# Optimization experiments

Measured on AMD Instinct MI355X. Metric: run time of the kernel, lower is better.

Reference implementation:

```python
import jax, jax.numpy as jnp
import numpy as np
import math

B, S, D, H, L, FF = 16, 512, 1024, 16, 4, 4096
DK = D // H
EPS = 1e-5
NEG = -1e32


def make_pe(max_len, d_model):
    pos = np.arange(max_len, dtype=np.float32)[:, None]
    div = np.exp(np.arange(0, d_model, 2, dtype=np.float32) * (-math.log(10000.0) / d_model))
    pe = np.zeros((max_len, d_model), dtype=np.float32)
    pe[:, 0::2] = np.sin(pos * div)
    pe[:, 1::2] = np.cos(pos * div)
    return jnp.asarray(pe[None])  # [1, max_len, d_model]


def setup_inputs() -> dict:
    key = jax.random.key(0)
    ks = jax.random.split(key, 32)
    sd = 0.02
    inp = {
        'q_embed_data': jax.random.normal(ks[0], (B, S, D), jnp.float32),
        'qa_embed_data': jax.random.normal(ks[1], (B, S, D), jnp.float32),
        'forget_rate': jax.random.uniform(ks[2], (B, 1, S, 1), jnp.float32),
        'pe': make_pe(S, D),
        'Wk': jax.random.normal(ks[3], (L, D, D), jnp.float32) * sd,
        'bk': jnp.zeros((L, D), jnp.float32),
        'Wv': jax.random.normal(ks[4], (L, D, D), jnp.float32) * sd,
        'bv': jnp.zeros((L, D), jnp.float32),
        'Wo': jax.random.normal(ks[5], (L, D, D), jnp.float32) * sd,
        'bo': jnp.zeros((L, D), jnp.float32),
        'W1': jax.random.normal(ks[6], (L, D, FF), jnp.float32) * sd,
        'b1': jnp.zeros((L, FF), jnp.float32),
        'W2': jax.random.normal(ks[7], (L, FF, D), jnp.float32) * sd,
        'b2': jnp.zeros((L, D), jnp.float32),
        'ln1_g': jnp.ones((L, D), jnp.float32),
        'ln1_b': jnp.zeros((L, D), jnp.float32),
        'ln2_g': jnp.ones((L, D), jnp.float32),
        'ln2_b': jnp.zeros((L, D), jnp.float32),
    }
    return inp


def layernorm(x, g, b):
    m = jnp.mean(x, -1, keepdims=True)
    v = jnp.mean((x - m) ** 2, -1, keepdims=True)
    return (x - m) * jax.lax.rsqrt(v + EPS) * g + b


def forward(q_embed_data, qa_embed_data, forget_rate, pe,
            Wk, bk, Wv, bv, Wo, bo, W1, b1, W2, b2,
            ln1_g, ln1_b, ln2_g, ln2_b):
    x = q_embed_data + pe[:, :S]
    y = qa_embed_data + pe[:, :S]
    # mask==0 path: allowed positions are strictly below diagonal (j < i)
    allowed = jnp.tril(jnp.ones((S, S), bool), k=-1)
    scale = 1.0 / math.sqrt(DK)
    for l in range(L):
        # kq_same: q also uses k_linear
        k = (x @ Wk[l] + bk[l]).reshape(B, S, H, DK).transpose(0, 2, 1, 3)
        q = k
        v = (y @ Wv[l] + bv[l]).reshape(B, S, H, DK).transpose(0, 2, 1, 3)
        scores = jnp.einsum('bhid,bhjd->bhij', q, k) * scale
        scores = scores * forget_rate  # [B,1,S,1] broadcasts over heads/cols
        scores = jnp.where(allowed, scores, NEG)
        attn = jax.nn.softmax(scores, axis=-1)
        attn = attn.at[:, :, 0, :].set(0.0)  # zero_pad of first query row
        out = jnp.einsum('bhij,bhjd->bhid', attn, v)
        out = out.transpose(0, 2, 1, 3).reshape(B, S, D) @ Wo[l] + bo[l]
        x = layernorm(x + out, ln1_g[l], ln1_b[l])
        ff = jax.nn.relu(x @ W1[l] + b1[l]) @ W2[l] + b2[l]
        x = layernorm(x + ff, ln2_g[l], ln2_b[l])
    return x


def reference(q_embed_data, qa_embed_data, forget_rate, pe,
              Wk, bk, Wv, bv, Wo, bo, W1, b1, W2, b2,
              ln1_g, ln1_b, ln2_g, ln2_b):
    return forward(q_embed_data, qa_embed_data, forget_rate, pe,
                   Wk, bk, Wv, bv, Wo, bo, W1, b1, W2, b2,
                   ln1_g, ln1_b, ln2_g, ln2_b)
```

## Files before the change

### kernel.cpp

```cpp
#include <hip/hip_runtime.h>
#include <hip/hip_bf16.h>
#include <cstdint>
#include <cstddef>

#define Bq 16
#define Sq 512
#define Dq 1024
#define Hq 16
#define Lq 4
#define FFq 4096
#define Mq (Bq * Sq)

typedef unsigned short ushort_t;
typedef __attribute__((ext_vector_type(8))) short short8;
typedef __attribute__((ext_vector_type(8))) unsigned short ushortx8;
typedef __attribute__((ext_vector_type(4))) unsigned short ushortx4;
typedef __attribute__((ext_vector_type(4))) float floatx4;

__device__ __forceinline__ float bf2f(ushort_t u) {
  union { unsigned int i; float f; } x;
  x.i = ((unsigned int)u) << 16;
  return x.f;
}
__device__ __forceinline__ ushort_t f2bf(float f) {
  unsigned int u = __float_as_uint(f);
  u += 0x7fffu + ((u >> 16) & 1u);
  return (ushort_t)(u >> 16);
}

#define GLL16(gp, lp) __builtin_amdgcn_global_load_lds( \
    (__attribute__((address_space(1))) void*)(gp),      \
    (__attribute__((address_space(3))) void*)(lp), 16, 0, 0)

__global__ void probe_kernel(const ushort_t* __restrict__ pe,
                             const ushort_t* __restrict__ g1,
                             int* __restrict__ flags)
{
  if (threadIdx.x == 0 && blockIdx.x == 0) {
    flags[0] = (pe[1] == (ushort_t)0x3F80u) ? 1 : 0;
    flags[1] = (g1[0] == (ushort_t)0x3F80u) ? 1 : 0;
  }
}

struct CvtArgs {
  const void* src[10];
  ushort_t*   dst[10];
  int         n[10];
  int         fi[10];
  int         cum[11];
};
__global__ __launch_bounds__(256) void convert_all_kernel(
    CvtArgs a, const int* __restrict__ flags)
{
  const int bidx = blockIdx.x;
  int s = 0;
  while (s < 9 && bidx >= a.cum[s + 1]) ++s;
  const int i = (bidx - a.cum[s]) * 256 + threadIdx.x;
  if (i >= a.n[s]) return;
  if (flags[a.fi[s]]) a.dst[s][i] = ((const ushort_t*)a.src[s])[i];
  else                a.dst[s][i] = f2bf(((const float*)a.src[s])[i]);
}

__global__ __launch_bounds__(256) void gemm_bt_kernel(
    const ushort_t* __restrict__ A0, const ushort_t* __restrict__ BT0,
    const ushort_t* __restrict__ bias0, ushort_t* __restrict__ C0,
    const ushort_t* __restrict__ A1, const ushort_t* __restrict__ BT1,
    const ushort_t* __restrict__ bias1, ushort_t* __restrict__ C1,
    int N, int K, int relu)
{
  __shared__ __align__(16) ushort_t As[2][128 * 32];
  __shared__ __align__(16) ushort_t Bs[2][64 * 32];

  const ushort_t* A    = blockIdx.z ? A1 : A0;
  const ushort_t* BT   = blockIdx.z ? BT1 : BT0;
  const ushort_t* bias = blockIdx.z ? bias1 : bias0;
  ushort_t*       C    = blockIdx.z ? C1 : C0;

  const int t = threadIdx.x;
  const int lane = t & 63;
  const int w = t >> 6;
  const int la = lane & 15;
  const int lb = lane >> 4;

  int bx = blockIdx.x, by = blockIdx.y;
  {
    const int gx = gridDim.x, gy = gridDim.y;
    if ((gy & 7) == 0) {
      const int orig = by * gx + bx;
      const int xcd = orig & 7;
      const int local = orig >> 3;
      const int rows = gy >> 3;
      by = xcd * rows + local % rows;
      bx = local / rows;
    }
  }
  const long m0 = (long)by * 128;
  const long n0 = (long)bx * 64;
  const int nk = K >> 5;

  const int rA0 = t >> 2;
  const int rA1 = 64 + (t >> 2);
  const int cg  = t & 3;
  const int cA0 = (cg ^ ((rA0 >> 1) & 3)) << 3;
  const int cA1 = (cg ^ ((rA1 >> 1) & 3)) << 3;
  const ushort_t* gA0 = A + (m0 + rA0) * K + cA0;
  const ushort_t* gA1 = A + (m0 + rA1) * K + cA1;
  const ushort_t* gB0 = BT + (n0 + rA0) * K + cA0;
  const int loA0 = (w * 64) * 8;
  const int loA1 = (256 + w * 64) * 8;
  const int loB0 = (w * 64) * 8;

#define STAGE(buf, kt) do {                      \
    const long ko_ = (long)(kt) << 5;            \
    GLL16(gA0 + ko_, &As[(buf)][loA0]);          \
    GLL16(gA1 + ko_, &As[(buf)][loA1]);          \
    GLL16(gB0 + ko_, &Bs[(buf)][loB0]);          \
  } while (0)

  const floatx4 z4 = {0.f, 0.f, 0.f, 0.f};
  floatx4 acc[4][2];
#pragma unroll
  for (int i = 0; i < 4; ++i)
#pragma unroll
    for (int j = 0; j < 2; ++j) acc[i][j] = z4;

  STAGE(0, 0);
  __syncthreads();

  const int wm = (w >> 1) * 64;
  const int wn = (w & 1) * 32;
  int cur = 0;

  for (int kt = 0; kt < nk; ++kt) {
    if (kt + 1 < nk) STAGE(cur ^ 1, kt + 1);

    short8 af[4], bfr[2];
#pragma unroll
    for (int mf = 0; mf < 4; ++mf) {
      const int r = wm + mf * 16 + la;
      af[mf] = *(const short8*)&As[cur][r * 32 + ((lb ^ ((r >> 1) & 3)) << 3)];
    }
#pragma unroll
    for (int nf = 0; nf < 2; ++nf) {
      const int r = wn + nf * 16 + la;
      bfr[nf] = *(const short8*)&Bs[cur][r * 32 + ((lb ^ ((r >> 1) & 3)) << 3)];
    }
#pragma unroll
    for (int mf = 0; mf < 4; ++mf)
#pragma unroll
      for (int nf = 0; nf < 2; ++nf)
        acc[mf][nf] = __builtin_amdgcn_mfma_f32_16x16x32_bf16(af[mf], bfr[nf], acc[mf][nf], 0, 0, 0);

    __syncthreads();
    cur ^= 1;
  }
#undef STAGE

#pragma unroll
  for (int nf = 0; nf < 2; ++nf) {
    const long col = n0 + wn + nf * 16 + la;
    const float bsv = bf2f(bias[col]);
#pragma unroll
    for (int mf = 0; mf < 4; ++mf) {
      const long row = m0 + wm + mf * 16 + lb * 4;
      ushort_t* cp = C + row * N + col;
      const floatx4 v = acc[mf][nf];
#pragma unroll
      for (int r = 0; r < 4; ++r) {
        float x = v[r] + bsv;
        if (relu) x = fmaxf(x, 0.0f);
        cp[(long)r * N] = f2bf(x);
      }
    }
  }
}

__global__ __launch_bounds__(256) void attn_kernel(
    const ushort_t* __restrict__ kq, const ushort_t* __restrict__ vt,
    const ushort_t* __restrict__ fr, ushort_t* __restrict__ ao)
{
  __shared__ __align__(16) ushort_t P[4][64 * 72];
  const int t = threadIdx.x;
  const int lane = t & 63;
  const int w4 = t >> 6;
  const int wq = blockIdx.y * 4 + w4;
  const int b = blockIdx.x >> 4;
  const int h = blockIdx.x & 15;
  const int la = lane & 15;
  const int lb = lane >> 4;
  const int i0 = wq * 64;
  const long kbase = ((long)b * Sq) * Dq + h * 64;
  const long vbase = ((long)(b * Hq + h)) * (64L * Sq);

  short8 qf[4][2];
#pragma unroll
  for (int mf = 0; mf < 4; ++mf)
#pragma unroll
    for (int tt = 0; tt < 2; ++tt)
      qf[mf][tt] = *(const short8*)&kq[kbase + (long)(i0 + mf * 16 + la) * Dq + tt * 32 + lb * 8];

  float frs[4][4];
#pragma unroll
  for (int mf = 0; mf < 4; ++mf)
#pragma unroll
    for (int r = 0; r < 4; ++r)
      frs[mf][r] = 0.125f * bf2f(fr[b * Sq + i0 + mf * 16 + lb * 4 + r]);

  const floatx4 z4 = {0.f, 0.f, 0.f, 0.f};
  floatx4 o[4][4];
  float mrun[4][4], lrun[4][4];
#pragma unroll
  for (int mf = 0; mf < 4; ++mf)
#pragma unroll
    for (int x = 0; x < 4; ++x) {
      o[mf][x] = z4;
      mrun[mf][x] = -1e30f;
      lrun[mf][x] = 0.0f;
    }

  for (int jt = 0; jt <= wq; ++jt) {
    const int j0 = jt * 64;
    floatx4 s[4][4];
#pragma unroll
    for (int mf = 0; mf < 4; ++mf)
#pragma unroll
      for (int jf = 0; jf < 4; ++jf) s[mf][jf] = z4;

#pragma unroll
    for (int tt = 0; tt < 2; ++tt) {
      short8 kf[4];
#pragma unroll
      for (int jf = 0; jf < 4; ++jf)
        kf[jf] = *(const short8*)&kq[kbase + (long)(j0 + jf * 16 + la) * Dq + tt * 32 + lb * 8];
#pragma unroll
      for (int mf = 0; mf < 4; ++mf)
#pragma unroll
        for (int jf = 0; jf < 4; ++jf)
          s[mf][jf] = __builtin_amdgcn_mfma_f32_16x16x32_bf16(qf[mf][tt], kf[jf], s[mf][jf], 0, 0, 0);
    }

    const bool diag = (jt == wq);
#pragma unroll
    for (int mf = 0; mf < 4; ++mf)
#pragma unroll
      for (int jf = 0; jf < 4; ++jf)
#pragma unroll
        for (int r = 0; r < 4; ++r) {
          float x = s[mf][jf][r] * frs[mf][r];
          if (diag && (j0 + jf * 16 + la) >= (i0 + mf * 16 + lb * 4 + r)) x = -1e30f;
          s[mf][jf][r] = x;
        }

#pragma unroll
    for (int mf = 0; mf < 4; ++mf)
#pragma unroll
      for (int r = 0; r < 4; ++r) {
        float pm = fmaxf(fmaxf(s[mf][0][r], s[mf][1][r]), fmaxf(s[mf][2][r], s[mf][3][r]));
        pm = fmaxf(pm, __shfl_xor(pm, 1));
        pm = fmaxf(pm, __shfl_xor(pm, 2));
        pm = fmaxf(pm, __shfl_xor(pm, 4));
        pm = fmaxf(pm, __shfl_xor(pm, 8));
        const float mo = mrun[mf][r];
        const float mn = fmaxf(mo, pm);
        const float sc = __expf(mo - mn);
        mrun[mf][r] = mn;
        float rs = 0.0f;
#pragma unroll
        for (int jf = 0; jf < 4; ++jf) {
          const float p = __expf(s[mf][jf][r] - mn);
          s[mf][jf][r] = p;
          rs += p;
        }
        rs += __shfl_xor(rs, 1);
        rs += __shfl_xor(rs, 2);
        rs += __shfl_xor(rs, 4);
        rs += __shfl_xor(rs, 8);
        lrun[mf][r] = lrun[mf][r] * sc + rs;
#pragma unroll
        for (int df = 0; df < 4; ++df) o[mf][df][r] *= sc;
      }

#pragma unroll
    for (int mf = 0; mf < 4; ++mf)
#pragma unroll
      for (int jf = 0; jf < 4; ++jf)
#pragma unroll
        for (int r = 0; r < 4; ++r)
          P[w4][(mf * 16 + lb * 4 + r) * 72 + jf * 16 + la] = f2bf(s[mf][jf][r]);

#pragma unroll
    for (int tt = 0; tt < 2; ++tt) {
      short8 pf[4], vf[4];
#pragma unroll
      for (int mf = 0; mf < 4; ++mf)
        pf[mf] = *(const short8*)&P[w4][(mf * 16 + la) * 72 + tt * 32 + lb * 8];
#pragma unroll
      for (int df = 0; df < 4; ++df)
        vf[df] = *(const short8*)&vt[vbase + (long)(df * 16 + la) * Sq + j0 + tt * 32 + lb * 8];
#pragma unroll
      for (int mf = 0; mf < 4; ++mf)
#pragma unroll
        for (int df = 0; df < 4; ++df)
          o[mf][df] = __builtin_amdgcn_mfma_f32_16x16x32_bf16(pf[mf], vf[df], o[mf][df], 0, 0, 0);
    }
  }

#pragma unroll
  for (int mf = 0; mf < 4; ++mf)
#pragma unroll
    for (int df = 0; df < 4; ++df)
#pragma unroll
      for (int r = 0; r < 4; ++r) {
        const int ii = i0 + mf * 16 + lb * 4 + r;
        const float vv = (ii == 0) ? 0.0f : o[mf][df][r] / lrun[mf][r];
        ao[((long)b * Sq + ii) * Dq + h * 64 + df * 16 + la] = f2bf(vv);
      }
}

__global__ __launch_bounds__(256) void ln_kernel(
    float* __restrict__ xf, const ushort_t* __restrict__ add,
    const ushort_t* __restrict__ g, const ushort_t* __restrict__ bb,
    ushort_t* __restrict__ outb, float* __restrict__ outf,
    const int* __restrict__ flags, int final_)
{
  __shared__ float red[2][4];
  const long row = blockIdx.x;
  const int t = threadIdx.x;
  const int c = t * 4;
  float* xr = xf + row * Dq;
  const ushort_t* ar = add + row * Dq;

  floatx4 xv = *(floatx4*)&xr[c];
  ushortx4 av = *(const ushortx4*)&ar[c];
  float v[4];
  float s1 = 0.f, s2 = 0.f;
#pragma unroll
  for (int e = 0; e < 4; ++e) {
    v[e] = xv[e] + bf2f(av[e]);
    s1 += v[e];
    s2 += v[e] * v[e];
  }
#pragma unroll
  for (int m = 1; m < 64; m <<= 1) {
    s1 += __shfl_xor(s1, m);
    s2 += __shfl_xor(s2, m);
  }
  const int lane = t & 63, w = t >> 6;
  if (lane == 0) { red[0][w] = s1; red[1][w] = s2; }
  __syncthreads();
  s1 = red[0][0] + red[0][1] + red[0][2] + red[0][3];
  s2 = red[1][0] + red[1][1] + red[1][2] + red[1][3];
  const float mean = s1 * (1.0f / Dq);
  const float var = fmaxf(s2 * (1.0f / Dq) - mean * mean, 0.0f);
  const float rstd = rsqrtf(var + 1e-5f);
  ushortx4 gv = *(const ushortx4*)&g[c];
  ushortx4 bv = *(const ushortx4*)&bb[c];
  ushortx4 ob;
  floatx4 xo;
#pragma unroll
  for (int e = 0; e < 4; ++e) {
    const float y = (v[e] - mean) * rstd * bf2f(gv[e]) + bf2f(bv[e]);
    xo[e] = y;
    ob[e] = f2bf(y);
  }
  *(floatx4*)&xr[c] = xo;
  if (final_ && !flags[0]) {
    *(floatx4*)&outf[row * Dq + c] = xo;
  } else {
    *(ushortx4*)&outb[row * Dq + c] = ob;
  }
}

__global__ __launch_bounds__(256) void addpe_kernel(
    const void* __restrict__ qe, const void* __restrict__ qa,
    const void* __restrict__ pe, float* __restrict__ xf,
    ushort_t* __restrict__ xb, ushort_t* __restrict__ yb,
    const int* __restrict__ flags)
{
  const long i = ((long)blockIdx.x * 256 + threadIdx.x) * 8;
  const long sd = i & ((long)Sq * Dq - 1);
  const bool isb = flags[0] != 0;
  float q[8], a[8], p[8];
  if (isb) {
    ushortx8 q8 = *(const ushortx8*)((const ushort_t*)qe + i);
    ushortx8 a8 = *(const ushortx8*)((const ushort_t*)qa + i);
    ushortx8 p8 = *(const ushortx8*)((const ushort_t*)pe + sd);
#pragma unroll
    for (int e = 0; e < 8; ++e) { q[e] = bf2f(q8[e]); a[e] = bf2f(a8[e]); p[e] = bf2f(p8[e]); }
  } else {
    const float* qp = (const float*)qe + i;
    const float* ap = (const float*)qa + i;
    const float* pp = (const float*)pe + sd;
    floatx4 q0 = *(const floatx4*)qp, q1 = *(const floatx4*)(qp + 4);
    floatx4 a0 = *(const floatx4*)ap, a1 = *(const floatx4*)(ap + 4);
    floatx4 p0 = *(const floatx4*)pp, p1 = *(const floatx4*)(pp + 4);
#pragma unroll
    for (int e = 0; e < 4; ++e) {
      q[e] = q0[e]; q[e + 4] = q1[e];
      a[e] = a0[e]; a[e + 4] = a1[e];
      p[e] = p0[e]; p[e + 4] = p1[e];
    }
  }
  ushortx8 xo, yo;
  floatx4 f0, f1;
#pragma unroll
  for (int e = 0; e < 8; ++e) {
    const float xvv = (isb ? q[e] : bf2f(f2bf(q[e]))) + (isb ? p[e] : bf2f(f2bf(p[e])));
    const float yvv = (isb ? a[e] : bf2f(f2bf(a[e]))) + (isb ? p[e] : bf2f(f2bf(p[e])));
    if (e < 4) { f0[e] = xvv; } else { f1[e - 4] = xvv; }
    xo[e] = f2bf(xvv);
    yo[e] = f2bf(yvv);
  }
  *(floatx4*)&xf[i] = f0;
  *(floatx4*)&xf[i + 4] = f1;
  *(ushortx8*)&xb[i] = xo;
  *(ushortx8*)&yb[i] = yo;
}

__global__ __launch_bounds__(256) void transpose_kernel(
    const void* __restrict__ src, ushort_t* __restrict__ dst, int K, int N,
    const int* __restrict__ flags)
{
  __shared__ __align__(16) ushort_t tile[64][72];
  const bool isb = flags[1] != 0;
  const long base = (long)blockIdx.z * K * N;
  const int k0 = blockIdx.y * 64, n0 = blockIdx.x * 64;
  const int t = threadIdx.x;
  const int r = t >> 3;
  const int cc = (t & 7) << 3;
#pragma unroll
  for (int it = 0; it < 2; ++it) {
    const int rr = r + it * 32;
    const long gi = base + (long)(k0 + rr) * N + n0 + cc;
    if (isb) {
      *(short8*)&tile[rr][cc] = *(const short8*)((const ushort_t*)src + gi);
    } else {
      const float* sf = (const float*)src + gi;
      floatx4 v0 = *(const floatx4*)sf;
      floatx4 v1 = *(const floatx4*)(sf + 4);
#pragma unroll
      for (int e = 0; e < 4; ++e) {
        tile[rr][cc + e] = f2bf(v0[e]);
        tile[rr][cc + 4 + e] = f2bf(v1[e]);
      }
    }
  }
  __syncthreads();
#pragma unroll
  for (int it = 0; it < 2; ++it) {
    const int rr = r + it * 32;
    short8 v;
#pragma unroll
    for (int e = 0; e < 8; ++e) v[e] = (short)tile[cc + e][rr];
    *(short8*)&dst[base + (long)(n0 + rr) * K + k0 + cc] = v;
  }
}

__global__ __launch_bounds__(256) void vtrans_kernel(
    const ushort_t* __restrict__ vb, ushort_t* __restrict__ vt)
{
  __shared__ __align__(16) ushort_t tile[64][72];
  const int b = blockIdx.y >> 4, h = blockIdx.y & 15;
  const int j0 = blockIdx.x * 64;
  const int t = threadIdx.x;
  const int r = t >> 3;
  const int cc = (t & 7) << 3;
#pragma unroll
  for (int it = 0; it < 2; ++it) {
    const int rr = r + it * 32;
    *(short8*)&tile[rr][cc] = *(const short8*)&vb[((long)b * Sq + j0 + rr) * Dq + h * 64 + cc];
  }
  __syncthreads();
#pragma unroll
  for (int it = 0; it < 2; ++it) {
    const int rr = r + it * 32;
    short8 v;
#pragma unroll
    for (int e = 0; e < 8; ++e) v[e] = (short)tile[cc + e][rr];
    *(short8*)&vt[((long)(b * Hq + h) * 64 + rr) * Sq + j0 + cc] = v;
  }
}

extern "C" void kernel_launch(void* const* d_in, const int* in_sizes, int n_in,
                              void* d_out, int out_size, void* d_ws, size_t ws_size,
                              hipStream_t stream)
{
  if (n_in < 18) return;
  const void* qe  = d_in[0];
  const void* qa  = d_in[1];
  const void* fr  = d_in[2];
  const void* pe  = d_in[3];
  const void* Wk  = d_in[4];
  const void* bk  = d_in[5];
  const void* Wv  = d_in[6];
  const void* bv  = d_in[7];
  const void* Wo  = d_in[8];
  const void* bo  = d_in[9];
  const void* W1  = d_in[10];
  const void* b1  = d_in[11];
  const void* W2  = d_in[12];
  const void* b2  = d_in[13];
  const void* g1  = d_in[14];
  const void* be1 = d_in[15];
  const void* g2  = d_in[16];
  const void* be2 = d_in[17];

  char* ws = (char*)d_ws;
  const size_t SM = 243269632L;
  const size_t NEED = SM + 114752L;
  if (ws_size < NEED) return;

  float*    xf   = (float*)   (ws + 0L);
  ushort_t* xb   = (ushort_t*)(ws + 33554432L);
  ushort_t* yb   = (ushort_t*)(ws + 50331648L);
  ushort_t* tmpD = (ushort_t*)(ws + 67108864L);
  ushort_t* WkT  = (ushort_t*)(ws + 83886080L);
  ushort_t* WvT  = (ushort_t*)(ws + 92274688L);
  ushort_t* WoT  = (ushort_t*)(ws + 100663296L);
  ushort_t* W1T  = (ushort_t*)(ws + 109051904L);
  ushort_t* W2T  = (ushort_t*)(ws + 142606336L);
  ushort_t* kb   = (ushort_t*)(ws + 176160768L);
  ushort_t* vbf  = (ushort_t*)(ws + 192937984L);
  ushort_t* vtb  = (ushort_t*)(ws + 209715200L);
  ushort_t* ff1  = kb;

  int*      flags = (int*)(ws + SM);
  ushort_t* frc  = (ushort_t*)(ws + SM + 64);
  ushort_t* bkc  = (ushort_t*)(ws + SM + 16448);
  ushort_t* bvc  = (ushort_t*)(ws + SM + 24640);
  ushort_t* boc  = (ushort_t*)(ws + SM + 32832);
  ushort_t* b1c  = (ushort_t*)(ws + SM + 41024);
  ushort_t* b2c  = (ushort_t*)(ws + SM + 73792);
  ushort_t* g1c  = (ushort_t*)(ws + SM + 81984);
  ushort_t* be1c = (ushort_t*)(ws + SM + 90176);
  ushort_t* g2c  = (ushort_t*)(ws + SM + 98368);
  ushort_t* be2c = (ushort_t*)(ws + SM + 106560);

  probe_kernel<<<1, 64, 0, stream>>>((const ushort_t*)pe, (const ushort_t*)g1, flags);

  {
    CvtArgs a;
    const void* srcs[10] = {fr, bk, bv, bo, b1, b2, g1, be1, g2, be2};
    ushort_t*   dsts[10] = {frc, bkc, bvc, boc, b1c, b2c, g1c, be1c, g2c, be2c};
    const int   ns[10]   = {8192, 4096, 4096, 4096, 16384, 4096, 4096, 4096, 4096, 4096};
    int cum = 0;
    for (int s = 0; s < 10; ++s) {
      a.src[s] = srcs[s]; a.dst[s] = dsts[s]; a.n[s] = ns[s];
      a.fi[s] = (s == 0) ? 0 : 1;
      a.cum[s] = cum;
      cum += (ns[s] + 255) / 256;
    }
    a.cum[10] = cum;
    convert_all_kernel<<<cum, 256, 0, stream>>>(a, flags);
  }

  transpose_kernel<<<dim3(16, 16, 4), 256, 0, stream>>>(Wk, WkT, 1024, 1024, flags);
  transpose_kernel<<<dim3(16, 16, 4), 256, 0, stream>>>(Wv, WvT, 1024, 1024, flags);
  transpose_kernel<<<dim3(16, 16, 4), 256, 0, stream>>>(Wo, WoT, 1024, 1024, flags);
  transpose_kernel<<<dim3(64, 16, 4), 256, 0, stream>>>(W1, W1T, 1024, 4096, flags);
  transpose_kernel<<<dim3(16, 64, 4), 256, 0, stream>>>(W2, W2T, 4096, 1024, flags);

  addpe_kernel<<<4096, 256, 0, stream>>>(qe, qa, pe, xf, xb, yb, flags);

  for (int l = 0; l < 4; ++l) {
    gemm_bt_kernel<<<dim3(16, 64, 2), 256, 0, stream>>>(
        xb, WkT + (long)l * 1048576, bkc + l * 1024, kb,
        yb, WvT + (long)l * 1048576, bvc + l * 1024, vbf,
        1024, 1024, 0);
    vtrans_kernel<<<dim3(8, 256), 256, 0, stream>>>(vbf, vtb);
    attn_kernel<<<dim3(256, 2), 256, 0, stream>>>(kb, vtb, frc, vbf);
    gemm_bt_kernel<<<dim3(16, 64, 1), 256, 0, stream>>>(
        vbf, WoT + (long)l * 1048576, boc + l * 1024, tmpD,
        vbf, WoT + (long)l * 1048576, boc + l * 1024, tmpD,
        1024, 1024, 0);
    ln_kernel<<<8192, 256, 0, stream>>>(xf, tmpD, g1c + l * 1024, be1c + l * 1024, xb, nullptr, flags, 0);
    gemm_bt_kernel<<<dim3(64, 64, 1), 256, 0, stream>>>(
        xb, W1T + (long)l * 4194304, b1c + l * 4096, ff1,
        xb, W1T + (long)l * 4194304, b1c + l * 4096, ff1,
        4096, 1024, 1);
    gemm_bt_kernel<<<dim3(16, 64, 1), 256, 0, stream>>>(
        ff1, W2T + (long)l * 4194304, b2c + l * 1024, tmpD,
        ff1, W2T + (long)l * 4194304, b2c + l * 1024, tmpD,
        1024, 4096, 0);
    if (l == 3) {
      ln_kernel<<<8192, 256, 0, stream>>>(xf, tmpD, g2c + l * 1024, be2c + l * 1024,
                                          (ushort_t*)d_out, (float*)d_out, flags, 1);
    } else {
      ln_kernel<<<8192, 256, 0, stream>>>(xf, tmpD, g2c + l * 1024, be2c + l * 1024,
                                          xb, nullptr, flags, 0);
    }
  }
}
```

Measured before the change: 1.790 ms.

## Replace GEMM with 8-wave 256xBN tiled kernel using ping-pong MFMA scheduling

```diff
diff --git a/kernel.cpp b/kernel.cpp
--- a/kernel.cpp
+++ b/kernel.cpp
@@ -31,6 +31,12 @@
 #define GLL16(gp, lp) __builtin_amdgcn_global_load_lds( \
     (__attribute__((address_space(1))) void*)(gp),      \
     (__attribute__((address_space(3))) void*)(lp), 16, 0, 0)
+
+template<int N> __device__ __forceinline__ void waitvm() {
+  if constexpr (N == 0)      asm volatile("s_waitcnt vmcnt(0)" ::: "memory");
+  else if constexpr (N == 6) asm volatile("s_waitcnt vmcnt(6)" ::: "memory");
+  else                       asm volatile("s_waitcnt vmcnt(8)" ::: "memory");
+}
 
 __global__ void probe_kernel(const ushort_t* __restrict__ pe,
                              const ushort_t* __restrict__ g1,
@@ -61,15 +67,29 @@
   else                a.dst[s][i] = f2bf(((const float*)a.src[s])[i]);
 }
 
-__global__ __launch_bounds__(256) void gemm_bt_kernel(
+template<int BN>
+__global__ __launch_bounds__(512) void gemm8p_kernel(
     const ushort_t* __restrict__ A0, const ushort_t* __restrict__ BT0,
     const ushort_t* __restrict__ bias0, ushort_t* __restrict__ C0,
     const ushort_t* __restrict__ A1, const ushort_t* __restrict__ BT1,
     const ushort_t* __restrict__ bias1, ushort_t* __restrict__ C1,
     int N, int K, int relu)
 {
-  __shared__ __align__(16) ushort_t As[2][128 * 32];
-  __shared__ __align__(16) ushort_t Bs[2][64 * 32];
+  constexpr int BM  = 256;
+  constexpr int CHA = 4;
+  constexpr int CHB = BN / 64;
+  constexpr int NVM = CHA + CHB;
+  constexpr int WC  = (BN == 256) ? 4 : 2;
+  constexpr int WR  = 8 / WC;
+  constexpr int WM  = BM / WR;
+  constexpr int WN  = BN / WC;
+  constexpr int MF  = WM / 16;
+  constexpr int NF  = WN / 16;
+  constexpr int MH  = MF / 2;
+  constexpr int NH  = NF / 2;
+
+  __shared__ __align__(16) ushort_t As[2][BM * 64];
+  __shared__ __align__(16) ushort_t Bs[2][BN * 64];
 
   const ushort_t* A    = blockIdx.z ? A1 : A0;
   const ushort_t* BT   = blockIdx.z ? BT1 : BT0;
@@ -78,9 +98,12 @@
 
   const int t = threadIdx.x;
   const int lane = t & 63;
-  const int w = t >> 6;
+  const int wid = t >> 6;
   const int la = lane & 15;
   const int lb = lane >> 4;
+  const int l7 = la & 7;
+  const int wr = wid / WC;
+  const int wc = wid % WC;
 
   int bx = blockIdx.x, by = blockIdx.y;
   {
@@ -94,75 +117,114 @@
       bx = local / rows;
     }
   }
-  const long m0 = (long)by * 128;
-  const long n0 = (long)bx * 64;
-  const int nk = K >> 5;
-
-  const int rA0 = t >> 2;
-  const int rA1 = 64 + (t >> 2);
-  const int cg  = t & 3;
-  const int cA0 = (cg ^ ((rA0 >> 1) & 3)) << 3;
-  const int cA1 = (cg ^ ((rA1 >> 1) & 3)) << 3;
-  const ushort_t* gA0 = A + (m0 + rA0) * K + cA0;
-  const ushort_t* gA1 = A + (m0 + rA1) * K + cA1;
-  const ushort_t* gB0 = BT + (n0 + rA0) * K + cA0;
-  const int loA0 = (w * 64) * 8;
-  const int loA1 = (256 + w * 64) * 8;
-  const int loB0 = (w * 64) * 8;
-
-#define STAGE(buf, kt) do {                      \
-    const long ko_ = (long)(kt) << 5;            \
-    GLL16(gA0 + ko_, &As[(buf)][loA0]);          \
-    GLL16(gA1 + ko_, &As[(buf)][loA1]);          \
-    GLL16(gB0 + ko_, &Bs[(buf)][loB0]);          \
+  const long m0 = (long)by * BM;
+  const long n0 = (long)bx * BN;
+  const int nkt = K >> 6;
+
+  const int srow = t >> 3;
+  const int scol = ((t & 7) ^ ((t >> 3) & 7)) << 3;
+  const ushort_t* sA = A + (m0 + srow) * K + scol;
+  const ushort_t* sB = BT + (n0 + srow) * K + scol;
+  const long chs = 64L * K;
+  const int ldsb = wid * 512;
+
+  const int cofs0 = ((0 * 4 + lb) ^ l7) << 3;
+  const int cofs1 = ((1 * 4 + lb) ^ l7) << 3;
+  const int arow = wr * WM + la;
+  const int brow = wc * WN + la;
+
+  floatx4 acc[MF][NF];
+#pragma unroll
+  for (int i = 0; i < MF; ++i)
+#pragma unroll
+    for (int j = 0; j < NF; ++j) acc[i][j] = (floatx4){0.f, 0.f, 0.f, 0.f};
+
+  short8 a[MH][2], b[NH][2];
+
+#define STG(kt_) do {                                                        \
+    const long ko_ = (long)(kt_) << 6;                                       \
+    ushort_t* asb = &As[(kt_) & 1][0];                                       \
+    ushort_t* bsb = &Bs[(kt_) & 1][0];                                       \
+    _Pragma("unroll")                                                        \
+    for (int c = 0; c < CHA; ++c) GLL16(sA + c * chs + ko_, asb + c * 4096 + ldsb); \
+    _Pragma("unroll")                                                        \
+    for (int c = 0; c < CHB; ++c) GLL16(sB + c * chs + ko_, bsb + c * 4096 + ldsb); \
   } while (0)
 
-  const floatx4 z4 = {0.f, 0.f, 0.f, 0.f};
-  floatx4 acc[4][2];
-#pragma unroll
-  for (int i = 0; i < 4; ++i)
-#pragma unroll
-    for (int j = 0; j < 2; ++j) acc[i][j] = z4;
-
-  STAGE(0, 0);
-  __syncthreads();
-
-  const int wm = (w >> 1) * 64;
-  const int wn = (w & 1) * 32;
-  int cur = 0;
-
-  for (int kt = 0; kt < nk; ++kt) {
-    if (kt + 1 < nk) STAGE(cur ^ 1, kt + 1);
-
-    short8 af[4], bfr[2];
-#pragma unroll
-    for (int mf = 0; mf < 4; ++mf) {
-      const int r = wm + mf * 16 + la;
-      af[mf] = *(const short8*)&As[cur][r * 32 + ((lb ^ ((r >> 1) & 3)) << 3)];
-    }
-#pragma unroll
-    for (int nf = 0; nf < 2; ++nf) {
-      const int r = wn + nf * 16 + la;
-      bfr[nf] = *(const short8*)&Bs[cur][r * 32 + ((lb ^ ((r >> 1) & 3)) << 3)];
-    }
-#pragma unroll
-    for (int mf = 0; mf < 4; ++mf)
-#pragma unroll
-      for (int nf = 0; nf < 2; ++nf)
-        acc[mf][nf] = __builtin_amdgcn_mfma_f32_16x16x32_bf16(af[mf], bfr[nf], acc[mf][nf], 0, 0, 0);
-
-    __syncthreads();
-    cur ^= 1;
-  }
-#undef STAGE
-
-#pragma unroll
-  for (int nf = 0; nf < 2; ++nf) {
-    const long col = n0 + wn + nf * 16 + la;
+#define RDA(mh_, bb_) do {                                                   \
+    _Pragma("unroll")                                                        \
+    for (int m2 = 0; m2 < MH; ++m2) {                                        \
+      const int r_ = arow + ((mh_) * MH + m2) * 16;                          \
+      a[m2][0] = *(const short8*)&As[bb_][r_ * 64 + cofs0];                  \
+      a[m2][1] = *(const short8*)&As[bb_][r_ * 64 + cofs1];                  \
+    } } while (0)
+
+#define RDB(nh_, bb_) do {                                                   \
+    _Pragma("unroll")                                                        \
+    for (int n2 = 0; n2 < NH; ++n2) {                                        \
+      const int r_ = brow + ((nh_) * NH + n2) * 16;                          \
+      b[n2][0] = *(const short8*)&Bs[bb_][r_ * 64 + cofs0];                  \
+      b[n2][1] = *(const short8*)&Bs[bb_][r_ * 64 + cofs1];                  \
+    } } while (0)
+
+#define MM(mh_, nh_) do {                                                    \
+    __builtin_amdgcn_s_setprio(1);                                           \
+    _Pragma("unroll")                                                        \
+    for (int m2 = 0; m2 < MH; ++m2)                                          \
+    _Pragma("unroll")                                                        \
+    for (int n2 = 0; n2 < NH; ++n2)                                          \
+    _Pragma("unroll")                                                        \
+    for (int kk = 0; kk < 2; ++kk)                                           \
+      acc[(mh_) * MH + m2][(nh_) * NH + n2] =                                \
+        __builtin_amdgcn_mfma_f32_16x16x32_bf16(                             \
+          a[m2][kk], b[n2][kk], acc[(mh_) * MH + m2][(nh_) * NH + n2], 0, 0, 0); \
+    __builtin_amdgcn_s_setprio(0);                                           \
+  } while (0)
+
+#define LGKM() do { asm volatile("s_waitcnt lgkmcnt(0)" ::: "memory");       \
+    __builtin_amdgcn_sched_barrier(0); } while (0)
+#define BAR() __builtin_amdgcn_s_barrier()
+
+  STG(0);
+  for (int kt = 0; kt < nkt; ++kt) {
+    const int bb = kt & 1;
+    if (kt + 1 < nkt) { STG(kt + 1); waitvm<NVM>(); }
+    else              { waitvm<0>(); }
+    BAR();
+    RDA(0, bb); RDB(0, bb);
+    LGKM();
+    MM(0, 0);
+    BAR();
+    RDB(1, bb);
+    BAR();
+    LGKM();
+    MM(0, 1);
+    BAR();
+    RDA(1, bb);
+    BAR();
+    LGKM();
+    MM(1, 1);
+    BAR();
+    RDB(0, bb);
+    BAR();
+    LGKM();
+    MM(1, 0);
+    BAR();
+  }
+#undef STG
+#undef RDA
+#undef RDB
+#undef MM
+#undef LGKM
+#undef BAR
+
+#pragma unroll
+  for (int nf = 0; nf < NF; ++nf) {
+    const long col = n0 + wc * WN + nf * 16 + la;
     const float bsv = bf2f(bias[col]);
 #pragma unroll
-    for (int mf = 0; mf < 4; ++mf) {
-      const long row = m0 + wm + mf * 16 + lb * 4;
+    for (int mf = 0; mf < MF; ++mf) {
+      const long row = m0 + wr * WM + mf * 16 + lb * 4;
       ushort_t* cp = C + row * N + col;
       const floatx4 v = acc[mf][nf];
 #pragma unroll
@@ -563,22 +625,22 @@
   addpe_kernel<<<4096, 256, 0, stream>>>(qe, qa, pe, xf, xb, yb, flags);
 
   for (int l = 0; l < 4; ++l) {
-    gemm_bt_kernel<<<dim3(16, 64, 2), 256, 0, stream>>>(
+    gemm8p_kernel<128><<<dim3(8, 32, 2), 512, 0, stream>>>(
         xb, WkT + (long)l * 1048576, bkc + l * 1024, kb,
         yb, WvT + (long)l * 1048576, bvc + l * 1024, vbf,
         1024, 1024, 0);
     vtrans_kernel<<<dim3(8, 256), 256, 0, stream>>>(vbf, vtb);
     attn_kernel<<<dim3(256, 2), 256, 0, stream>>>(kb, vtb, frc, vbf);
-    gemm_bt_kernel<<<dim3(16, 64, 1), 256, 0, stream>>>(
+    gemm8p_kernel<128><<<dim3(8, 32, 1), 512, 0, stream>>>(
         vbf, WoT + (long)l * 1048576, boc + l * 1024, tmpD,
         vbf, WoT + (long)l * 1048576, boc + l * 1024, tmpD,
         1024, 1024, 0);
     ln_kernel<<<8192, 256, 0, stream>>>(xf, tmpD, g1c + l * 1024, be1c + l * 1024, xb, nullptr, flags, 0);
-    gemm_bt_kernel<<<dim3(64, 64, 1), 256, 0, stream>>>(
+    gemm8p_kernel<256><<<dim3(16, 32, 1), 512, 0, stream>>>(
         xb, W1T + (long)l * 4194304, b1c + l * 4096, ff1,
         xb, W1T + (long)l * 4194304, b1c + l * 4096, ff1,
         4096, 1024, 1);
-    gemm_bt_kernel<<<dim3(16, 64, 1), 256, 0, stream>>>(
+    gemm8p_kernel<128><<<dim3(8, 32, 1), 512, 0, stream>>>(
         ff1, W2T + (long)l * 4194304, b2c + l * 1024, tmpD,
         ff1, W2T + (long)l * 4194304, b2c + l * 1024, tmpD,
         1024, 4096, 0);
```

After: 1.920 ms. 1.07x slower.

## Enlarge GEMM tile to 256x128 with explicit vmcnt-pipelined double buffering

Applied to the files above, without the earlier changes.

```diff
diff --git a/kernel.cpp b/kernel.cpp
--- a/kernel.cpp
+++ b/kernel.cpp
@@ -61,15 +61,15 @@
   else                a.dst[s][i] = f2bf(((const float*)a.src[s])[i]);
 }
 
-__global__ __launch_bounds__(256) void gemm_bt_kernel(
+__global__ __launch_bounds__(256, 2) void gemmw_kernel(
     const ushort_t* __restrict__ A0, const ushort_t* __restrict__ BT0,
     const ushort_t* __restrict__ bias0, ushort_t* __restrict__ C0,
     const ushort_t* __restrict__ A1, const ushort_t* __restrict__ BT1,
     const ushort_t* __restrict__ bias1, ushort_t* __restrict__ C1,
     int N, int K, int relu)
 {
-  __shared__ __align__(16) ushort_t As[2][128 * 32];
-  __shared__ __align__(16) ushort_t Bs[2][64 * 32];
+  __shared__ __align__(16) ushort_t As[2][256 * 32];
+  __shared__ __align__(16) ushort_t Bs[2][128 * 32];
 
   const ushort_t* A    = blockIdx.z ? A1 : A0;
   const ushort_t* BT   = blockIdx.z ? BT1 : BT0;
@@ -78,9 +78,11 @@
 
   const int t = threadIdx.x;
   const int lane = t & 63;
-  const int w = t >> 6;
+  const int wid = t >> 6;
   const int la = lane & 15;
   const int lb = lane >> 4;
+  const int wr = wid >> 1;
+  const int wc = wid & 1;
 
   int bx = blockIdx.x, by = blockIdx.y;
   {
@@ -94,75 +96,75 @@
       bx = local / rows;
     }
   }
-  const long m0 = (long)by * 128;
-  const long n0 = (long)bx * 64;
+  const long m0 = (long)by * 256;
+  const long n0 = (long)bx * 128;
   const int nk = K >> 5;
 
-  const int rA0 = t >> 2;
-  const int rA1 = 64 + (t >> 2);
-  const int cg  = t & 3;
-  const int cA0 = (cg ^ ((rA0 >> 1) & 3)) << 3;
-  const int cA1 = (cg ^ ((rA1 >> 1) & 3)) << 3;
-  const ushort_t* gA0 = A + (m0 + rA0) * K + cA0;
-  const ushort_t* gA1 = A + (m0 + rA1) * K + cA1;
-  const ushort_t* gB0 = BT + (n0 + rA0) * K + cA0;
-  const int loA0 = (w * 64) * 8;
-  const int loA1 = (256 + w * 64) * 8;
-  const int loB0 = (w * 64) * 8;
-
-#define STAGE(buf, kt) do {                      \
-    const long ko_ = (long)(kt) << 5;            \
-    GLL16(gA0 + ko_, &As[(buf)][loA0]);          \
-    GLL16(gA1 + ko_, &As[(buf)][loA1]);          \
-    GLL16(gB0 + ko_, &Bs[(buf)][loB0]);          \
+  const int rA = t >> 2;
+  const int scol = (((t & 3) ^ ((rA >> 1) & 3)) << 3);
+  const ushort_t* sA = A + (m0 + rA) * (long)K + scol;
+  const ushort_t* sB = BT + (n0 + rA) * (long)K + scol;
+  const long rs64 = 64L * (long)K;
+  const int lws = wid * 512;
+
+#define STG(buf_, kt_) do {                                  \
+    const long ko_ = (long)(kt_) << 5;                       \
+    GLL16(sA + ko_,            &As[(buf_)][lws]);            \
+    GLL16(sA + rs64 + ko_,     &As[(buf_)][2048 + lws]);     \
+    GLL16(sA + 2 * rs64 + ko_, &As[(buf_)][4096 + lws]);     \
+    GLL16(sA + 3 * rs64 + ko_, &As[(buf_)][6144 + lws]);     \
+    GLL16(sB + ko_,            &Bs[(buf_)][lws]);            \
+    GLL16(sB + rs64 + ko_,     &Bs[(buf_)][2048 + lws]);     \
   } while (0)
 
-  const floatx4 z4 = {0.f, 0.f, 0.f, 0.f};
-  floatx4 acc[4][2];
-#pragma unroll
-  for (int i = 0; i < 4; ++i)
-#pragma unroll
-    for (int j = 0; j < 2; ++j) acc[i][j] = z4;
-
-  STAGE(0, 0);
-  __syncthreads();
-
-  const int wm = (w >> 1) * 64;
-  const int wn = (w & 1) * 32;
-  int cur = 0;
+  floatx4 acc[8][4];
+#pragma unroll
+  for (int i = 0; i < 8; ++i)
+#pragma unroll
+    for (int j = 0; j < 4; ++j) acc[i][j] = (floatx4){0.f, 0.f, 0.f, 0.f};
+
+  const int cofs = ((lb ^ ((la >> 1) & 3)) << 3);
+  const int ar0 = wr * 128 + la;
+  const int br0 = wc * 64 + la;
+
+  STG(0, 0);
 
   for (int kt = 0; kt < nk; ++kt) {
-    if (kt + 1 < nk) STAGE(cur ^ 1, kt + 1);
-
-    short8 af[4], bfr[2];
-#pragma unroll
-    for (int mf = 0; mf < 4; ++mf) {
-      const int r = wm + mf * 16 + la;
-      af[mf] = *(const short8*)&As[cur][r * 32 + ((lb ^ ((r >> 1) & 3)) << 3)];
-    }
-#pragma unroll
-    for (int nf = 0; nf < 2; ++nf) {
-      const int r = wn + nf * 16 + la;
-      bfr[nf] = *(const short8*)&Bs[cur][r * 32 + ((lb ^ ((r >> 1) & 3)) << 3)];
-    }
-#pragma unroll
-    for (int mf = 0; mf < 4; ++mf)
-#pragma unroll
-      for (int nf = 0; nf < 2; ++nf)
-        acc[mf][nf] = __builtin_amdgcn_mfma_f32_16x16x32_bf16(af[mf], bfr[nf], acc[mf][nf], 0, 0, 0);
-
-    __syncthreads();
-    cur ^= 1;
-  }
-#undef STAGE
-
-#pragma unroll
-  for (int nf = 0; nf < 2; ++nf) {
-    const long col = n0 + wn + nf * 16 + la;
+    const int buf = kt & 1;
+    if (kt + 1 < nk) {
+      STG(buf ^ 1, kt + 1);
+      asm volatile("s_waitcnt vmcnt(6)" ::: "memory");
+    } else {
+      asm volatile("s_waitcnt vmcnt(0)" ::: "memory");
+    }
+    __builtin_amdgcn_s_barrier();
+    __builtin_amdgcn_sched_barrier(0);
+
+    short8 af[8], bf[4];
+#pragma unroll
+    for (int mf = 0; mf < 8; ++mf)
+      af[mf] = *(const short8*)&As[buf][(ar0 + mf * 16) * 32 + cofs];
+#pragma unroll
+    for (int nf = 0; nf < 4; ++nf)
+      bf[nf] = *(const short8*)&Bs[buf][(br0 + nf * 16) * 32 + cofs];
+
+#pragma unroll
+    for (int nf = 0; nf < 4; ++nf)
+#pragma unroll
+      for (int mf = 0; mf < 8; ++mf)
+        acc[mf][nf] = __builtin_amdgcn_mfma_f32_16x16x32_bf16(af[mf], bf[nf], acc[mf][nf], 0, 0, 0);
+
+    __builtin_amdgcn_s_barrier();
+  }
+#undef STG
+
+#pragma unroll
+  for (int nf = 0; nf < 4; ++nf) {
+    const long col = n0 + wc * 64 + nf * 16 + la;
     const float bsv = bf2f(bias[col]);
 #pragma unroll
-    for (int mf = 0; mf < 4; ++mf) {
-      const long row = m0 + wm + mf * 16 + lb * 4;
+    for (int mf = 0; mf < 8; ++mf) {
+      const long row = m0 + wr * 128 + mf * 16 + lb * 4;
       ushort_t* cp = C + row * N + col;
       const floatx4 v = acc[mf][nf];
 #pragma unroll
@@ -563,22 +565,22 @@
   addpe_kernel<<<4096, 256, 0, stream>>>(qe, qa, pe, xf, xb, yb, flags);
 
   for (int l = 0; l < 4; ++l) {
-    gemm_bt_kernel<<<dim3(16, 64, 2), 256, 0, stream>>>(
+    gemmw_kernel<<<dim3(8, 32, 2), 256, 0, stream>>>(
         xb, WkT + (long)l * 1048576, bkc + l * 1024, kb,
         yb, WvT + (long)l * 1048576, bvc + l * 1024, vbf,
         1024, 1024, 0);
     vtrans_kernel<<<dim3(8, 256), 256, 0, stream>>>(vbf, vtb);
     attn_kernel<<<dim3(256, 2), 256, 0, stream>>>(kb, vtb, frc, vbf);
-    gemm_bt_kernel<<<dim3(16, 64, 1), 256, 0, stream>>>(
+    gemmw_kernel<<<dim3(8, 32, 1), 256, 0, stream>>>(
         vbf, WoT + (long)l * 1048576, boc + l * 1024, tmpD,
         vbf, WoT + (long)l * 1048576, boc + l * 1024, tmpD,
         1024, 1024, 0);
     ln_kernel<<<8192, 256, 0, stream>>>(xf, tmpD, g1c + l * 1024, be1c + l * 1024, xb, nullptr, flags, 0);
-    gemm_bt_kernel<<<dim3(64, 64, 1), 256, 0, stream>>>(
+    gemmw_kernel<<<dim3(32, 32, 1), 256, 0, stream>>>(
         xb, W1T + (long)l * 4194304, b1c + l * 4096, ff1,
         xb, W1T + (long)l * 4194304, b1c + l * 4096, ff1,
         4096, 1024, 1);
-    gemm_bt_kernel<<<dim3(16, 64, 1), 256, 0, stream>>>(
+    gemmw_kernel<<<dim3(8, 32, 1), 256, 0, stream>>>(
         ff1, W2T + (long)l * 4194304, b2c + l * 1024, tmpD,
         ff1, W2T + (long)l * 4194304, b2c + l * 1024, tmpD,
         1024, 4096, 0);
```

Measured after the change: 1.816 ms. No clear change (+1.4%).
